# Optimization experiments

Hardware: AMD Instinct MI355X
Metric: run time of the kernel (lower is better)

## Reference

```python
import jax, jax.numpy as jnp
import numpy as np

HEADS = 12  # hard-coded in the original module (rearrange h=12, temp shape (12,1))


def setup_inputs() -> dict:
    key = jax.random.key(0)
    k1, k2, k3 = jax.random.split(key, 3)
    B, C, H, W = 16, 768, 64, 64  # C = 3*dim with dim=256; per-head d = C/12 = 64
    x = jax.random.normal(k1, (B, C, H, W), dtype=jnp.float32)
    W_qkv = jax.random.normal(k2, (C, C), dtype=jnp.float32) * 0.02
    W_out = jax.random.normal(k3, (C, C), dtype=jnp.float32) * 0.02
    temp = jnp.ones((HEADS, 1), dtype=jnp.float32)
    return {"x": x, "W_qkv": W_qkv, "W_out": W_out, "temp": temp}


def reference(x, W_qkv, W_out, temp):
    B, C, H, W = x.shape
    N = H * W
    d = C // HEADS
    # to_3d: b c h w -> b (h w) c
    x3 = jnp.transpose(x, (0, 2, 3, 1)).reshape(B, N, C)
    # qkv projection (nn.Linear, no bias): x @ W^T
    w = (x3 @ W_qkv.T).reshape(B, N, HEADS, d).transpose(0, 2, 1, 3)  # [B, H, N, d]
    # F.normalize along the token axis (dim=-2), eps=1e-12
    norm = jnp.sqrt(jnp.sum(w * w, axis=2, keepdims=True))
    w_normed = w / jnp.maximum(norm, 1e-12)
    w_sq = w_normed ** 2
    # per-(head, token) stats, scaled by learned temp, softmax over HEADS axis (dim=1!)
    logits = jnp.sum(w_sq, axis=-1) * temp          # [B, H, N] (temp [12,1] broadcasts)
    Pi = jax.nn.softmax(logits, axis=1)             # softmax over heads
    Pi_n = Pi / (jnp.sum(Pi, axis=-1, keepdims=True) + 1e-8)
    # dots: [B,H,1,N] @ [B,H,N,d] -> [B,H,1,d]
    dots = jnp.einsum('bhn,bhnd->bhd', Pi_n, w ** 2)[:, :, None, :]
    attn = 1.0 / (1.0 + dots)                       # [B, H, 1, d]
    out = -(w * Pi[..., None]) * attn               # [B, H, N, d]
    # b h n d -> b n (h d)
    out = out.transpose(0, 2, 1, 3).reshape(B, N, C)
    out = out @ W_out.T
    # b (h w) c -> b c h w
    return out.reshape(B, H, W, C).transpose(0, 3, 1, 2)
```

## Files before the change

kernel.cpp:

```cpp
#include <hip/hip_runtime.h>
#include <stdint.h>

#define B_ 16
#define C_ 768
#define N_ 4096
#define HEADS_ 12

typedef __attribute__((ext_vector_type(4))) float f32x4;
typedef __attribute__((ext_vector_type(8))) short s16x8;

__device__ __forceinline__ ushort f2bf(float f){
  union { float f; uint32_t u; } v; v.f = f;
  uint32_t u = v.u;
  uint32_t r = (u + 0x7fffu + ((u >> 16) & 1u)) >> 16;
  return (ushort)r;
}
__device__ __forceinline__ float bf2f(ushort h){
  union { uint32_t u; float f; } v; v.u = ((uint32_t)h) << 16;
  return v.f;
}

__device__ __forceinline__ void gload16(const ushort* g, ushort* l){
  __builtin_amdgcn_global_load_lds(
      (__attribute__((address_space(1))) void*)(g),
      (__attribute__((address_space(3))) void*)(l), 16, 0, 0);
}

__global__ __launch_bounds__(256) void k_convert(const float* __restrict__ src,
                                                 ushort* __restrict__ dst, int n){
  int i = (blockIdx.x * 256 + threadIdx.x) * 4;
  if (i < n){
    float4 v = *(const float4*)(src + i);
    ushort4 u;
    u.x = f2bf(v.x); u.y = f2bf(v.y); u.z = f2bf(v.z); u.w = f2bf(v.w);
    *(ushort4*)(dst + i) = u;
  }
}

__global__ __launch_bounds__(256) void k_transpose(const float* __restrict__ x,
                                                   ushort* __restrict__ xT){
  __shared__ ushort tile[64][72];
  int b = blockIdx.z;
  int n0 = blockIdx.x * 64;
  int k0 = blockIdx.y * 64;
  int t = threadIdx.x;
  const float* xb = x + (size_t)b * C_ * N_;
  #pragma unroll
  for (int p = 0; p < 4; ++p){
    int krow = (t >> 4) + p * 16;
    int nn = (t & 15) * 4;
    float4 v = *(const float4*)(xb + (size_t)(k0 + krow) * N_ + n0 + nn);
    tile[nn + 0][krow] = f2bf(v.x);
    tile[nn + 1][krow] = f2bf(v.y);
    tile[nn + 2][krow] = f2bf(v.z);
    tile[nn + 3][krow] = f2bf(v.w);
  }
  __syncthreads();
  ushort* dst = xT + (size_t)b * N_ * C_;
  #pragma unroll
  for (int p = 0; p < 4; ++p){
    int nrow = (t >> 4) + p * 16;
    int kk = (t & 15) * 4;
    ushort4 u = *(ushort4*)&tile[nrow][kk];
    *(ushort4*)(dst + (size_t)(n0 + nrow) * C_ + k0 + kk) = u;
  }
}

#define BM 128
#define BN 128
#define BK 64

__global__ __launch_bounds__(256, 2) void k_gemm1(const ushort* __restrict__ xT,
                                                  const ushort* __restrict__ wq,
                                                  ushort* __restrict__ w,
                                                  float* __restrict__ colnorm2){
  __shared__ ushort As[BM * BK];
  __shared__ ushort Bs[BN * BK];
  int b = blockIdx.z;
  int n0 = blockIdx.x * BM;
  int c0 = blockIdx.y * BN;
  int t = threadIdx.x;
  int lane = t & 63, wv = t >> 6;
  int wm = wv >> 1, wn = wv & 1;
  int col = lane & 15, quad = lane >> 4;
  const ushort* Ag = xT + (size_t)b * N_ * C_ + (size_t)n0 * C_;
  const ushort* Bg = wq + (size_t)c0 * C_;
  int srow = lane >> 3;
  int sch  = (lane & 7) * 8;
  f32x4 acc[4][4] = {};
  for (int kt = 0; kt < C_; kt += BK){
    #pragma unroll
    for (int c = 0; c < 4; ++c){
      int rb8 = wv * 32 + c * 8;
      int r = rb8 + srow;
      gload16(Ag + (size_t)r * C_ + kt + sch, &As[rb8 * 64]);
      gload16(Bg + (size_t)r * C_ + kt + sch, &Bs[rb8 * 64]);
    }
    __syncthreads();
    #pragma unroll
    for (int ks = 0; ks < 2; ++ks){
      s16x8 af[4], bfr[4];
      #pragma unroll
      for (int mt = 0; mt < 4; ++mt)
        af[mt] = *(const s16x8*)&As[(wm * 64 + mt * 16 + col) * 64 + ks * 32 + quad * 8];
      #pragma unroll
      for (int nt = 0; nt < 4; ++nt)
        bfr[nt] = *(const s16x8*)&Bs[(wn * 64 + nt * 16 + col) * 64 + ks * 32 + quad * 8];
      #pragma unroll
      for (int mt = 0; mt < 4; ++mt)
        #pragma unroll
        for (int nt = 0; nt < 4; ++nt)
          acc[mt][nt] = __builtin_amdgcn_mfma_f32_16x16x32_bf16(af[mt], bfr[nt], acc[mt][nt], 0, 0, 0);
    }
    __syncthreads();
  }
  ushort* wb = w + (size_t)b * N_ * C_;
  #pragma unroll
  for (int nt = 0; nt < 4; ++nt){
    int cc = c0 + wn * 64 + nt * 16 + col;
    float ss = 0.f;
    #pragma unroll
    for (int mt = 0; mt < 4; ++mt){
      #pragma unroll
      for (int r = 0; r < 4; ++r){
        int nn = n0 + wm * 64 + mt * 16 + quad * 4 + r;
        float v = acc[mt][nt][r];
        wb[(size_t)nn * C_ + cc] = f2bf(v);
        ss += v * v;
      }
    }
    ss += __shfl_xor(ss, 16);
    ss += __shfl_xor(ss, 32);
    if (quad == 0) atomicAdd(colnorm2 + b * C_ + cc, ss);
  }
}

__global__ __launch_bounds__(256) void k_stats(ushort* __restrict__ w,
                                               const float* __restrict__ colnorm2,
                                               const float* __restrict__ temp,
                                               float* __restrict__ S,
                                               float* __restrict__ T){
  int b = blockIdx.y;
  int chunk = blockIdx.x;
  int t = threadIdx.x;
  int lane = t & 63, wv = t >> 6;
  float invcn[HEADS_], tmp[HEADS_], S_loc[HEADS_], T_loc[HEADS_];
  #pragma unroll
  for (int j = 0; j < HEADS_; ++j){
    float cn = colnorm2[b * C_ + j * 64 + lane];
    invcn[j] = 1.0f / fmaxf(cn, 1e-24f);
    tmp[j] = temp[j];
    S_loc[j] = 0.f; T_loc[j] = 0.f;
  }
  ushort* wb = w + (size_t)b * N_ * C_;
  for (int it = 0; it < 32; ++it){
    int n = chunk * 128 + wv * 32 + it;
    ushort* row = wb + (size_t)n * C_;
    float fj[HEADS_], r[HEADS_];
    #pragma unroll
    for (int j = 0; j < HEADS_; ++j){
      float f = bf2f(row[j * 64 + lane]);
      fj[j] = f;
      r[j] = f * f * invcn[j];
    }
    #pragma unroll
    for (int j = 0; j < HEADS_; ++j){
      #pragma unroll
      for (int off = 1; off < 64; off <<= 1)
        r[j] += __shfl_xor(r[j], off);
    }
    float m = -1e30f;
    #pragma unroll
    for (int j = 0; j < HEADS_; ++j){ r[j] *= tmp[j]; m = fmaxf(m, r[j]); }
    float se = 0.f, p[HEADS_];
    #pragma unroll
    for (int j = 0; j < HEADS_; ++j){ p[j] = __expf(r[j] - m); se += p[j]; }
    float inv = 1.0f / se;
    #pragma unroll
    for (int j = 0; j < HEADS_; ++j){
      p[j] *= inv;
      S_loc[j] += p[j];
      T_loc[j] += p[j] * fj[j] * fj[j];
      row[j * 64 + lane] = f2bf(fj[j] * p[j]);
    }
  }
  #pragma unroll
  for (int j = 0; j < HEADS_; ++j){
    atomicAdd(T + b * C_ + j * 64 + lane, T_loc[j]);
    if (lane == j) atomicAdd(S + b * HEADS_ + j, S_loc[j]);
  }
}

__global__ __launch_bounds__(256) void k_scale_wout(const float* __restrict__ Wout,
                                                    const float* __restrict__ S,
                                                    const float* __restrict__ T,
                                                    ushort* __restrict__ woS,
                                                    int b0){
  int bz = blockIdx.y; int b = b0 + bz;
  int i = (blockIdx.x * 256 + threadIdx.x) * 4;
  int k = i % C_;
  float s = S[b * HEADS_ + (k >> 6)] + 1e-8f;
  float4 t4 = *(const float4*)(T + b * C_ + k);
  float4 v = *(const float4*)(Wout + i);
  ushort4 u;
  u.x = f2bf(-v.x * s / (s + t4.x));
  u.y = f2bf(-v.y * s / (s + t4.y));
  u.z = f2bf(-v.z * s / (s + t4.z));
  u.w = f2bf(-v.w * s / (s + t4.w));
  *(ushort4*)(woS + (size_t)bz * C_ * C_ + i) = u;
}

__global__ __launch_bounds__(256, 2) void k_gemm2(const ushort* __restrict__ wp,
                                                  const ushort* __restrict__ woS,
                                                  float* __restrict__ out,
                                                  int b0){
  __shared__ ushort As[BM * BK];
  __shared__ ushort Bs[BN * BK];
  int bz = blockIdx.z; int b = b0 + bz;
  int c0 = blockIdx.x * BM;
  int n0 = blockIdx.y * BN;
  int t = threadIdx.x;
  int lane = t & 63, wv = t >> 6;
  int wm = wv >> 1, wn = wv & 1;
  int col = lane & 15, quad = lane >> 4;
  const ushort* Ag = woS + (size_t)bz * C_ * C_ + (size_t)c0 * C_;
  const ushort* Bg = wp + (size_t)b * N_ * C_ + (size_t)n0 * C_;
  int srow = lane >> 3;
  int sch  = (lane & 7) * 8;
  f32x4 acc[4][4] = {};
  for (int kt = 0; kt < C_; kt += BK){
    #pragma unroll
    for (int c = 0; c < 4; ++c){
      int rb8 = wv * 32 + c * 8;
      int r = rb8 + srow;
      gload16(Ag + (size_t)r * C_ + kt + sch, &As[rb8 * 64]);
      gload16(Bg + (size_t)r * C_ + kt + sch, &Bs[rb8 * 64]);
    }
    __syncthreads();
    #pragma unroll
    for (int ks = 0; ks < 2; ++ks){
      s16x8 af[4], bfr[4];
      #pragma unroll
      for (int mt = 0; mt < 4; ++mt)
        af[mt] = *(const s16x8*)&As[(wm * 64 + mt * 16 + col) * 64 + ks * 32 + quad * 8];
      #pragma unroll
      for (int nt = 0; nt < 4; ++nt)
        bfr[nt] = *(const s16x8*)&Bs[(wn * 64 + nt * 16 + col) * 64 + ks * 32 + quad * 8];
      #pragma unroll
      for (int mt = 0; mt < 4; ++mt)
        #pragma unroll
        for (int nt = 0; nt < 4; ++nt)
          acc[mt][nt] = __builtin_amdgcn_mfma_f32_16x16x32_bf16(af[mt], bfr[nt], acc[mt][nt], 0, 0, 0);
    }
    __syncthreads();
  }
  #pragma unroll
  for (int mt = 0; mt < 4; ++mt){
    #pragma unroll
    for (int nt = 0; nt < 4; ++nt){
      int nn = n0 + wn * 64 + nt * 16 + col;
      #pragma unroll
      for (int r = 0; r < 4; ++r){
        int cc = c0 + wm * 64 + mt * 16 + quad * 4 + r;
        out[((size_t)b * C_ + cc) * N_ + nn] = acc[mt][nt][r];
      }
    }
  }
}

extern "C" void kernel_launch(void* const* d_in, const int* in_sizes, int n_in,
                              void* d_out, int out_size, void* d_ws, size_t ws_size,
                              hipStream_t stream){
  const float* x    = (const float*)d_in[0];
  const float* Wqkv = (const float*)d_in[1];
  const float* Wout = (const float*)d_in[2];
  const float* temp = (const float*)d_in[3];
  float* out = (float*)d_out;
  char* ws = (char*)d_ws;

  const size_t sz_w     = (size_t)B_ * N_ * C_ * sizeof(ushort);
  const size_t sz_wt    = (size_t)C_ * C_ * sizeof(ushort);
  const size_t sz_stats = (size_t)(2 * B_ * C_ + B_ * HEADS_) * sizeof(float);

  ushort* w_buf    = (ushort*)ws;
  float*  colnorm2 = (float*)(ws + sz_w);
  float*  S_       = colnorm2 + B_ * C_;
  float*  T_       = S_ + B_ * HEADS_;
  ushort* woS      = (ushort*)(ws + sz_w + sz_stats);

  ushort* xT   = (ushort*)d_out;
  ushort* wq_b = (ushort*)((char*)d_out + sz_w);

  hipMemsetAsync(colnorm2, 0, sz_stats, stream);
  k_convert<<<576, 256, 0, stream>>>(Wqkv, wq_b, C_ * C_);
  k_transpose<<<dim3(N_ / 64, C_ / 64, B_), 256, 0, stream>>>(x, xT);
  k_gemm1<<<dim3(N_ / BM, C_ / BN, B_), 256, 0, stream>>>(xT, wq_b, w_buf, colnorm2);
  k_stats<<<dim3(32, B_), 256, 0, stream>>>(w_buf, colnorm2, temp, S_, T_);

  const size_t need_full = sz_w + sz_stats + (size_t)B_ * sz_wt;
  if (ws_size >= need_full){
    k_scale_wout<<<dim3(C_ * C_ / 1024, B_), 256, 0, stream>>>(Wout, S_, T_, woS, 0);
    k_gemm2<<<dim3(C_ / BM, N_ / BN, B_), 256, 0, stream>>>(w_buf, woS, out, 0);
  } else {
    for (int b0 = 0; b0 < B_; b0 += 4){
      k_scale_wout<<<dim3(C_ * C_ / 1024, 4), 256, 0, stream>>>(Wout, S_, T_, woS, b0);
      k_gemm2<<<dim3(C_ / BM, N_ / BN, 4), 256, 0, stream>>>(w_buf, woS, out, b0);
    }
  }
}
```

Measured before the change: 699.1 us.

## Vectorize stats kernel per-lane column layout and remap gemm2 blocks across XCDs

The stats kernel now gives each lane four contiguous bf16 columns, loaded and stored as ushort4. Head sums are reduced with 16-lane shuffles and then exchanged across lane groups, instead of a full 64-lane reduction per head for every row. This replaces scalar 2-byte accesses and many shuffles, and the launch grid is doubled to 64 chunks per batch of 64 rows each. The output GEMM remaps its linear block id so that neighbouring tiles are grouped onto the same XCD for better L2 reuse. The remap hard-codes the 6x32 tile grid per batch.

After: 662.2 us. -5.3%, faster.

```diff
diff --git a/kernel.cpp b/kernel.cpp
--- a/kernel.cpp
+++ b/kernel.cpp
@@ -144,50 +144,89 @@
   int chunk = blockIdx.x;
   int t = threadIdx.x;
   int lane = t & 63, wv = t >> 6;
-  float invcn[HEADS_], tmp[HEADS_], S_loc[HEADS_], T_loc[HEADS_];
-  #pragma unroll
-  for (int j = 0; j < HEADS_; ++j){
-    float cn = colnorm2[b * C_ + j * 64 + lane];
-    invcn[j] = 1.0f / fmaxf(cn, 1e-24f);
-    tmp[j] = temp[j];
-    S_loc[j] = 0.f; T_loc[j] = 0.f;
-  }
+  int g = lane >> 4;
+  int colb = (lane & 15) * 4;
+
+  float invcn[3][4], tval[3][4], T_loc[3][4], S_own[3];
+  #pragma unroll
+  for (int L = 0; L < 3; ++L){
+    float4 cn = *(const float4*)(colnorm2 + b * C_ + (4 * L + g) * 64 + colb);
+    invcn[L][0] = 1.0f / fmaxf(cn.x, 1e-24f);
+    invcn[L][1] = 1.0f / fmaxf(cn.y, 1e-24f);
+    invcn[L][2] = 1.0f / fmaxf(cn.z, 1e-24f);
+    invcn[L][3] = 1.0f / fmaxf(cn.w, 1e-24f);
+    #pragma unroll
+    for (int k = 0; k < 4; ++k) tval[L][k] = temp[4 * L + (g ^ k)];
+    #pragma unroll
+    for (int i = 0; i < 4; ++i) T_loc[L][i] = 0.f;
+    S_own[L] = 0.f;
+  }
+
   ushort* wb = w + (size_t)b * N_ * C_;
-  for (int it = 0; it < 32; ++it){
-    int n = chunk * 128 + wv * 32 + it;
+  for (int it = 0; it < 16; ++it){
+    int n = chunk * 64 + wv * 16 + it;
     ushort* row = wb + (size_t)n * C_;
-    float fj[HEADS_], r[HEADS_];
-    #pragma unroll
-    for (int j = 0; j < HEADS_; ++j){
-      float f = bf2f(row[j * 64 + lane]);
-      fj[j] = f;
-      r[j] = f * f * invcn[j];
-    }
-    #pragma unroll
-    for (int j = 0; j < HEADS_; ++j){
-      #pragma unroll
-      for (int off = 1; off < 64; off <<= 1)
-        r[j] += __shfl_xor(r[j], off);
-    }
-    float m = -1e30f;
-    #pragma unroll
-    for (int j = 0; j < HEADS_; ++j){ r[j] *= tmp[j]; m = fmaxf(m, r[j]); }
-    float se = 0.f, p[HEADS_];
-    #pragma unroll
-    for (int j = 0; j < HEADS_; ++j){ p[j] = __expf(r[j] - m); se += p[j]; }
+    float f[3][4], v[3][4], part[3];
+    #pragma unroll
+    for (int L = 0; L < 3; ++L){
+      ushort4 u = *(const ushort4*)(row + (lane + 64 * L) * 4);
+      f[L][0] = bf2f(u.x); f[L][1] = bf2f(u.y);
+      f[L][2] = bf2f(u.z); f[L][3] = bf2f(u.w);
+      part[L] = 0.f;
+      #pragma unroll
+      for (int i = 0; i < 4; ++i){
+        v[L][i] = f[L][i] * f[L][i];
+        part[L] += v[L][i] * invcn[L][i];
+      }
+    }
+    #pragma unroll
+    for (int L = 0; L < 3; ++L){
+      #pragma unroll
+      for (int off = 1; off < 16; off <<= 1)
+        part[L] += __shfl_xor(part[L], off);
+    }
+    float val[3][4];
+    #pragma unroll
+    for (int L = 0; L < 3; ++L){
+      val[L][0] = tval[L][0] * part[L];
+      val[L][1] = tval[L][1] * __shfl_xor(part[L], 16);
+      val[L][2] = tval[L][2] * __shfl_xor(part[L], 32);
+      val[L][3] = tval[L][3] * __shfl_xor(part[L], 48);
+    }
+    float m = val[0][0];
+    #pragma unroll
+    for (int L = 0; L < 3; ++L)
+      #pragma unroll
+      for (int k = 0; k < 4; ++k) m = fmaxf(m, val[L][k]);
+    float se = 0.f, e0[3];
+    #pragma unroll
+    for (int L = 0; L < 3; ++L){
+      #pragma unroll
+      for (int k = 0; k < 4; ++k){
+        float e = __expf(val[L][k] - m);
+        se += e;
+        if (k == 0) e0[L] = e;
+      }
+    }
     float inv = 1.0f / se;
     #pragma unroll
-    for (int j = 0; j < HEADS_; ++j){
-      p[j] *= inv;
-      S_loc[j] += p[j];
-      T_loc[j] += p[j] * fj[j] * fj[j];
-      row[j * 64 + lane] = f2bf(fj[j] * p[j]);
-    }
-  }
-  #pragma unroll
-  for (int j = 0; j < HEADS_; ++j){
-    atomicAdd(T + b * C_ + j * 64 + lane, T_loc[j]);
-    if (lane == j) atomicAdd(S + b * HEADS_ + j, S_loc[j]);
+    for (int L = 0; L < 3; ++L){
+      float p = e0[L] * inv;
+      S_own[L] += p;
+      ushort4 s4;
+      T_loc[L][0] += p * v[L][0];  s4.x = f2bf(f[L][0] * p);
+      T_loc[L][1] += p * v[L][1];  s4.y = f2bf(f[L][1] * p);
+      T_loc[L][2] += p * v[L][2];  s4.z = f2bf(f[L][2] * p);
+      T_loc[L][3] += p * v[L][3];  s4.w = f2bf(f[L][3] * p);
+      *(ushort4*)(row + (lane + 64 * L) * 4) = s4;
+    }
+  }
+  #pragma unroll
+  for (int L = 0; L < 3; ++L){
+    #pragma unroll
+    for (int i = 0; i < 4; ++i)
+      atomicAdd(T + b * C_ + (4 * L + g) * 64 + colb + i, T_loc[L][i]);
+    if ((lane & 15) == 0) atomicAdd(S + b * HEADS_ + 4 * L + g, S_own[L]);
   }
 }
 
@@ -216,14 +255,20 @@
                                                   int b0){
   __shared__ ushort As[BM * BK];
   __shared__ ushort Bs[BN * BK];
-  int bz = blockIdx.z; int b = b0 + bz;
-  int c0 = blockIdx.x * BM;
-  int n0 = blockIdx.y * BN;
+  int nwg = gridDim.x * gridDim.y * gridDim.z;
+  int hid = blockIdx.x + gridDim.x * (blockIdx.y + gridDim.y * blockIdx.z);
+  int lid = (hid & 7) * (nwg >> 3) + (hid >> 3);
+  int xb = lid % 6;
+  int yb = (lid / 6) % 32;
+  int zb = lid / 192;
+  int b = b0 + zb;
+  int c0 = xb * BM;
+  int n0 = yb * BN;
   int t = threadIdx.x;
   int lane = t & 63, wv = t >> 6;
   int wm = wv >> 1, wn = wv & 1;
   int col = lane & 15, quad = lane >> 4;
-  const ushort* Ag = woS + (size_t)bz * C_ * C_ + (size_t)c0 * C_;
+  const ushort* Ag = woS + (size_t)zb * C_ * C_ + (size_t)c0 * C_;
   const ushort* Bg = wp + (size_t)b * N_ * C_ + (size_t)n0 * C_;
   int srow = lane >> 3;
   int sch  = (lane & 7) * 8;
@@ -295,7 +340,7 @@
   k_convert<<<576, 256, 0, stream>>>(Wqkv, wq_b, C_ * C_);
   k_transpose<<<dim3(N_ / 64, C_ / 64, B_), 256, 0, stream>>>(x, xT);
   k_gemm1<<<dim3(N_ / BM, C_ / BN, B_), 256, 0, stream>>>(xT, wq_b, w_buf, colnorm2);
-  k_stats<<<dim3(32, B_), 256, 0, stream>>>(w_buf, colnorm2, temp, S_, T_);
+  k_stats<<<dim3(64, B_), 256, 0, stream>>>(w_buf, colnorm2, temp, S_, T_);
 
   const size_t need_full = sz_w + sz_stats + (size_t)B_ * sz_wt;
   if (ws_size >= need_full){
```
